# Optimization experiments

Measured on AMD Instinct MI355X. Metric: run time of the kernel, lower is better.

## Reference

```python
import jax, jax.numpy as jnp
import numpy as np

B, T, D, H, DEPTH, FF, NC = 512, 150, 256, 8, 6, 1024, 4
HD = D // H  # head dim = 32


def setup_inputs() -> dict:
    key = jax.random.key(0)
    ks = iter(jax.random.split(key, 64))
    n = lambda shape, s=0.02: jax.random.normal(next(ks), shape, jnp.float32) * s
    return dict(
        token_types=jax.random.randint(next(ks), (B, T), 0, 4, jnp.int32),
        decision_ids=jax.random.randint(next(ks), (B, T), 0, NC, jnp.int32),
        action_vals=jax.random.normal(next(ks), (B, T, 1), jnp.float32),
        dis_vals=jax.random.normal(next(ks), (B, T, 10), jnp.float32),
        v_vals=jax.random.normal(next(ks), (B, T, 3), jnp.float32),
        action_W=n((1, D), 0.5), action_b=n((D,)),
        dis_W=n((10, D), 0.2), dis_b=n((D,)),
        v_W=n((3, D), 0.3), v_b=n((D,)),
        decision_table=n((NC, D)),
        pos_embed=n((1, T + 1, D)), cls_token=n((1, 1, D)),
        qkv_W=n((DEPTH, D, 3 * D), 0.05), qkv_b=jnp.zeros((DEPTH, 3 * D), jnp.float32),
        out_W=n((DEPTH, D, D), 0.05), out_b=jnp.zeros((DEPTH, D), jnp.float32),
        ln1_g=jnp.ones((DEPTH, D), jnp.float32), ln1_b=jnp.zeros((DEPTH, D), jnp.float32),
        ln2_g=jnp.ones((DEPTH, D), jnp.float32), ln2_b=jnp.zeros((DEPTH, D), jnp.float32),
        ffn1_W=n((DEPTH, D, FF), 0.05), ffn1_b=jnp.zeros((DEPTH, FF), jnp.float32),
        ffn2_W=n((DEPTH, FF, D), 0.05), ffn2_b=jnp.zeros((DEPTH, D), jnp.float32),
        dec_ln_g=jnp.ones((D,), jnp.float32), dec_ln_b=jnp.zeros((D,), jnp.float32),
        dec_W=n((D, NC), 0.05), dec_b=jnp.zeros((NC,), jnp.float32),
        act_ln_g=jnp.ones((D,), jnp.float32), act_ln_b=jnp.zeros((D,), jnp.float32),
        act_W=n((D, 1), 0.05), act_b=jnpp if False else jnp.zeros((1,), jnp.float32),
    )


def _ln(x, g, b):
    # PyTorch LayerNorm: eps=1e-5, biased variance
    m = jnp.mean(x, axis=-1, keepdims=True)
    v = jnp.mean(jnp.square(x - m), axis=-1, keepdims=True)
    return (x - m) * jax.lax.rsqrt(v + 1e-5) * g + b


def reference(token_types, decision_ids, action_vals, dis_vals, v_vals,
              action_W, action_b, dis_W, dis_b, v_W, v_b, decision_table,
              pos_embed, cls_token, qkv_W, qkv_b, out_W, out_b,
              ln1_g, ln1_b, ln2_g, ln2_b, ffn1_W, ffn1_b, ffn2_W, ffn2_b,
              dec_ln_g, dec_ln_b, dec_W, dec_b, act_ln_g, act_ln_b, act_W, act_b):
    # --- batched type-dispatched token embedding (replaces the per-token python loop) ---
    a_emb = action_vals @ action_W + action_b                     # [B,T,D] type 'A'
    s_emb = dis_vals @ dis_W + dis_b + v_vals @ v_W + v_b         # [B,T,D] type 'S'
    d_emb = decision_table[decision_ids]                          # [B,T,D] type 'D'
    t = token_types[..., None]
    x = jnp.where(t == 0, a_emb, jnp.where(t == 1, s_emb, jnp.where(t == 2, d_emb, 0.0)))
    # --- prepend CLS, add positional embedding ---
    x = jnp.concatenate([jnp.broadcast_to(cls_token, (x.shape[0], 1, D)), x], axis=1)
    S = x.shape[1]
    x = x + pos_embed[:, :S, :]
    # --- post-norm TransformerEncoder (PyTorch default: ReLU FFN, norm_first=False, eval/no dropout) ---
    scale = 1.0 / np.sqrt(HD).astype(np.float32)
    for i in range(DEPTH):
        qkv = x @ qkv_W[i] + qkv_b[i]                             # [B,S,3D]
        q, k, v = jnp.split(qkv, 3, axis=-1)
        q = q.reshape(-1, S, H, HD)
        k = k.reshape(-1, S, H, HD)
        v = v.reshape(-1, S, H, HD)
        att = jax.nn.softmax(jnp.einsum('bqhd,bkhd->bhqk', q, k) * scale, axis=-1)
        o = jnp.einsum('bhqk,bkhd->bqhd', att, v).reshape(-1, S, D)
        x = _ln(x + o @ out_W[i] + out_b[i], ln1_g[i], ln1_b[i])
        ff = jax.nn.relu(x @ ffn1_W[i] + ffn1_b[i]) @ ffn2_W[i] + ffn2_b[i]
        x = _ln(x + ff, ln2_g[i], ln2_b[i])
    cls = x[:, 0, :]
    decision_logits = _ln(cls, dec_ln_g, dec_ln_b) @ dec_W + dec_b   # [B,4]
    action_pred = _ln(cls, act_ln_g, act_ln_b) @ act_W + act_b       # [B,1]
    return (decision_logits, action_pred)
```

## Files before the change

### kernel.cpp

```cpp
#include <hip/hip_runtime.h>
#include <hip/hip_bf16.h>

typedef __hip_bfloat16 bf16;
typedef unsigned short u16;
typedef __attribute__((ext_vector_type(8))) short s16x8;
typedef __attribute__((ext_vector_type(4))) float f32x4;

#define B_ 512
#define T_ 150
#define S_ 151
#define D_ 256
#define H_ 8
#define HD_ 32
#define FF_ 1024
#define NC_ 4
#define DEPTH_ 6
#define MTOT 77312
#define MT128 (MTOT / 128)
#define MT64 (MTOT / 64)

#define XOFF 0
#define C1OFF (MTOT * D_)
#define C2OFF (C1OFF + MTOT * FF_)
#define WSELEMS (C2OFF + MTOT * D_)

#define QKVT_OFF 0
#define OUTT_OFF (QKVT_OFF + DEPTH_ * D_ * 768)
#define FFN1T_OFF (OUTT_OFF + DEPTH_ * D_ * D_)
#define FFN2T_OFF (FFN1T_OFF + DEPTH_ * D_ * FF_)
#define WTELEMS (FFN2T_OFF + DEPTH_ * FF_ * D_)

__device__ __align__(16) u16 g_ws[WSELEMS];
__device__ __align__(16) u16 g_wt[WTELEMS];
__device__ int g_f32flag;

__device__ __forceinline__ float ldf(const void* p, size_t i, int f) {
  return f ? ((const float*)p)[i] : __bfloat162float(((const bf16*)p)[i]);
}
__device__ __forceinline__ float b2f(u16 u) {
  union { unsigned int i; float f; } v; v.i = ((unsigned int)u) << 16; return v.f;
}
__device__ __forceinline__ u16 f2b(float x) {
  bf16 h = __float2bfloat16(x);
  return *reinterpret_cast<u16*>(&h);
}

typedef __attribute__((address_space(3))) void lds_void;
typedef const __attribute__((address_space(1))) void glob_void;
__device__ __forceinline__ void gload_lds16(const u16* g, u16* l) {
  __builtin_amdgcn_global_load_lds((glob_void*)g, (lds_void*)l, 16, 0, 0);
}

#define PROBE_N 38656
__global__ __launch_bounds__(256) void probe_kernel(const void* pe)
{
  const u16* w = (const u16*)pe;
  int susp = 0, zeroEven = 0;
  for (int k = threadIdx.x; k < PROBE_N; k += 256) {
    u16 u = w[k];
    int ex = (u >> 7) & 0xFF;
    if (ex >= 141) susp++;
    if ((k & 1) == 0 && (u & 0x7FFF) == 0) zeroEven++;
  }
  __shared__ int s_susp, s_zero;
  if (threadIdx.x == 0) { s_susp = 0; s_zero = 0; }
  __syncthreads();
  atomicAdd(&s_susp, susp);
  atomicAdd(&s_zero, zeroEven);
  __syncthreads();
  if (threadIdx.x == 0)
    g_f32flag = (s_susp > 0 || s_zero >= ((PROBE_N / 2) * 9) / 10) ? 1 : 0;
}

__global__ __launch_bounds__(256) void wtrans_kernel(const void* src, int dstOff,
                                                     int K, int N, int total)
{
  const int f = g_f32flag;
  int idx = blockIdx.x * 256 + threadIdx.x;
  if (idx >= total) return;
  int kn = K * N;
  int l = idx / kn;
  int r = idx - l * kn;
  int k = r / N;
  int n = r - k * N;
  g_wt[dstOff + (size_t)l * kn + (size_t)n * K + k] = f2b(ldf(src, idx, f));
}

__global__ __launch_bounds__(256) void embed_kernel(
    const int* __restrict__ tt, const int* __restrict__ dids,
    const void* av, const void* dv, const void* vv,
    const void* aW, const void* ab, const void* dW, const void* db,
    const void* vW, const void* vb, const void* table, const void* pos,
    const void* cls)
{
  const int f = g_f32flag;
  u16* x = g_ws + XOFF;
  int row = blockIdx.x;
  int d = threadIdx.x;
  int b = row / S_;
  int s = row - b * S_;
  float val;
  if (s == 0) {
    val = ldf(cls, d, f);
  } else {
    int t = s - 1;
    int idx = b * T_ + t;
    int ty = tt[idx];
    if (ty == 0) {
      val = ldf(av, idx, f) * ldf(aW, d, f) + ldf(ab, d, f);
    } else if (ty == 1) {
      float acc = ldf(db, d, f) + ldf(vb, d, f);
#pragma unroll
      for (int i = 0; i < 10; i++) acc += ldf(dv, (size_t)idx * 10 + i, f) * ldf(dW, i * D_ + d, f);
#pragma unroll
      for (int i = 0; i < 3; i++) acc += ldf(vv, (size_t)idx * 3 + i, f) * ldf(vW, i * D_ + d, f);
      val = acc;
    } else if (ty == 2) {
      int did = dids[idx] & (NC_ - 1);
      val = ldf(table, (size_t)did * D_ + d, f);
    } else {
      val = 0.f;
    }
  }
  val += ldf(pos, s * D_ + d, f);
  x[(size_t)row * D_ + d] = f2b(val);
}

__global__ __launch_bounds__(256, 3) void gemm_mfma(
    int aOff, int wtOff, const void* bias, size_t bOff,
    int cOff, int N, int K, int relu, int NB)
{
  const int f = g_f32flag;
  const u16* A = g_ws + aOff;
  const u16* Bt = g_wt + wtOff;
  u16* C = g_ws + cOff;
  __shared__ __align__(16) u16 sm[16384];
  const int tid = threadIdx.x;

  int gblk = blockIdx.x;
  int bm, bn;
  {
    const int full = (MT128 / 8) * 8;
    if (gblk < NB * full) {
      int per = NB * 8;
      int grp = gblk / per, rem = gblk % per;
      bm = grp * 8 + (rem & 7);
      bn = rem >> 3;
    } else {
      int id = gblk - NB * full;
      bm = full + id / NB;
      bn = id % NB;
    }
  }

  const int lane = tid & 63, wid = tid >> 6;
  const int wm = (wid >> 1) * 64, wn = (wid & 1) * 64;
  const int frow = lane & 15, quad = lane >> 4;

  const int rg = lane >> 3;
  const int ck = ((lane & 7) ^ rg) * 8;
  const u16* Ag[4]; const u16* Bg[4];
  u16 *Asl[4], *Bsl[4];
#pragma unroll
  for (int p = 0; p < 4; p++) {
    int grp = wid * 4 + p;
    int row = grp * 8 + rg;
    Ag[p] = A + (size_t)(bm * 128 + row) * K + ck;
    Bg[p] = Bt + (size_t)(bn * 128 + row) * K + ck;
    Asl[p] = &sm[grp * 512];
    Bsl[p] = &sm[8192 + grp * 512];
  }

  f32x4 acc[4][4] = {};

  for (int kt = 0; kt < K; kt += 64) {
    if (kt) __syncthreads();
#pragma unroll
    for (int p = 0; p < 4; p++) {
      gload_lds16(Ag[p] + kt, Asl[p]);
      gload_lds16(Bg[p] + kt, Bsl[p]);
    }
    __syncthreads();
#pragma unroll
    for (int s = 0; s < 2; s++) {
      s16x8 af[4], bfr[4];
      const int cfr = ((s * 4 + quad) ^ (frow & 7)) * 8;
#pragma unroll
      for (int t = 0; t < 4; t++) {
        af[t]  = *(const s16x8*)&sm[(wm + t * 16 + frow) * 64 + cfr];
        bfr[t] = *(const s16x8*)&sm[8192 + (wn + t * 16 + frow) * 64 + cfr];
      }
#pragma unroll
      for (int mt = 0; mt < 4; mt++)
#pragma unroll
        for (int nt = 0; nt < 4; nt++)
          acc[mt][nt] = __builtin_amdgcn_mfma_f32_16x16x32_bf16(af[mt], bfr[nt], acc[mt][nt], 0, 0, 0);
    }
  }

  float bv[4];
#pragma unroll
  for (int nt = 0; nt < 4; nt++)
    bv[nt] = ldf(bias, bOff + (size_t)(bn * 128 + wn + nt * 16 + frow), f);
  __syncthreads();
#pragma unroll
  for (int p = 0; p < 2; p++) {
    if ((wid >> 1) == p) {
#pragma unroll
      for (int mt = 0; mt < 4; mt++)
#pragma unroll
        for (int nt = 0; nt < 4; nt++)
#pragma unroll
          for (int r = 0; r < 4; r++) {
            int rl = (wm & 63) + mt * 16 + quad * 4 + r;
            float v = acc[mt][nt][r] + bv[nt];
            if (relu) v = fmaxf(v, 0.f);
            sm[rl * 136 + wn + nt * 16 + frow] = f2b(v);
          }
    }
    __syncthreads();
    {
      int rl = tid >> 2;
      int cq = (tid & 3) * 32;
      size_t gb = (size_t)(bm * 128 + p * 64 + rl) * N + bn * 128 + cq;
#pragma unroll
      for (int j = 0; j < 4; j++)
        *(s16x8*)(C + gb + j * 8) = *(const s16x8*)&sm[rl * 136 + cq + j * 8];
    }
    __syncthreads();
  }
}

#define LNHALF 20480

__global__ __launch_bounds__(256, 2) void gemm_ln(
    int aOff, int wtOff, const void* bias, size_t bOff,
    const void* lng, const void* lnb, size_t lnOff, int K)
{
  const int f = g_f32flag;
  const u16* A = g_ws + aOff;
  const u16* Bt = g_wt + wtOff;
  __shared__ __align__(16) u16 sm[2 * LNHALF];
  const int tid = threadIdx.x;
  const int bm = blockIdx.x;
  const int lane = tid & 63, wid = tid >> 6;
  const int wn = wid * 64;
  const int frow = lane & 15, quad = lane >> 4;
  const int rg = lane >> 3;
  const int ck = ((lane & 7) ^ rg) * 8;

  const u16* Ag[2]; u16* Asl[2];
  const u16* Bg[8]; u16* Bsl[8];
#pragma unroll
  for (int p = 0; p < 2; p++) {
    int grp = wid * 2 + p;
    Ag[p] = A + (size_t)(bm * 64 + grp * 8 + rg) * K + ck;
    Asl[p] = &sm[grp * 512];
  }
#pragma unroll
  for (int p = 0; p < 8; p++) {
    int grp = wid * 8 + p;
    Bg[p] = Bt + (size_t)(grp * 8 + rg) * K + ck;
    Bsl[p] = &sm[4096 + grp * 512];
  }

  f32x4 acc[4][4] = {};
  const int nsteps = K >> 6;

#pragma unroll
  for (int p = 0; p < 2; p++) gload_lds16(Ag[p], Asl[p]);
#pragma unroll
  for (int p = 0; p < 8; p++) gload_lds16(Bg[p], Bsl[p]);
  __syncthreads();

  for (int t = 0; t < nsteps; t++) {
    const int cur = (t & 1) * LNHALF;
    if (t + 1 < nsteps) {
      const int nxt = ((t + 1) & 1) * LNHALF;
      const int kt = (t + 1) << 6;
#pragma unroll
      for (int p = 0; p < 2; p++) gload_lds16(Ag[p] + kt, Asl[p] + nxt);
#pragma unroll
      for (int p = 0; p < 8; p++) gload_lds16(Bg[p] + kt, Bsl[p] + nxt);
    }
#pragma unroll
    for (int s = 0; s < 2; s++) {
      s16x8 af[4], bfr[4];
      const int cfr = ((s * 4 + quad) ^ (frow & 7)) * 8;
#pragma unroll
      for (int ti = 0; ti < 4; ti++) {
        af[ti]  = *(const s16x8*)&sm[cur + (ti * 16 + frow) * 64 + cfr];
        bfr[ti] = *(const s16x8*)&sm[cur + 4096 + (wn + ti * 16 + frow) * 64 + cfr];
      }
#pragma unroll
      for (int mt = 0; mt < 4; mt++)
#pragma unroll
        for (int nt = 0; nt < 4; nt++)
          acc[mt][nt] = __builtin_amdgcn_mfma_f32_16x16x32_bf16(af[mt], bfr[nt], acc[mt][nt], 0, 0, 0);
    }
    __syncthreads();
  }

  const int rl = tid >> 2;
  const int cq = (tid & 3) * 64;
  const size_t rowg = (size_t)bm * 64 + rl;
  s16x8 xr[8];
#pragma unroll
  for (int j = 0; j < 8; j++)
    xr[j] = *(const s16x8*)(g_ws + XOFF + rowg * 256 + cq + j * 8);

  float bv[4];
#pragma unroll
  for (int nt = 0; nt < 4; nt++)
    bv[nt] = ldf(bias, bOff + (size_t)(wn + nt * 16 + frow), f);
#pragma unroll
  for (int mt = 0; mt < 4; mt++)
#pragma unroll
    for (int nt = 0; nt < 4; nt++)
#pragma unroll
      for (int r = 0; r < 4; r++) {
        int row = mt * 16 + quad * 4 + r;
        int col = wn + nt * 16 + frow;
        sm[row * 264 + col] = f2b(acc[mt][nt][r] + bv[nt]);
      }
  __syncthreads();
  {
    float s1 = 0.f, s2 = 0.f;
#pragma unroll
    for (int j = 0; j < 8; j++) {
      s16x8 yv = *(const s16x8*)&sm[rl * 264 + cq + j * 8];
#pragma unroll
      for (int e = 0; e < 8; e++) {
        float v = b2f((u16)yv[e]) + b2f((u16)xr[j][e]);
        s1 += v; s2 += v * v;
      }
    }
    s1 += __shfl_xor(s1, 1, 64); s2 += __shfl_xor(s2, 1, 64);
    s1 += __shfl_xor(s1, 2, 64); s2 += __shfl_xor(s2, 2, 64);
    float mean = s1 * (1.f / 256.f);
    float var = s2 * (1.f / 256.f) - mean * mean;
    float rs = rsqrtf(var + 1e-5f);
#pragma unroll
    for (int j = 0; j < 8; j++) {
      s16x8 yv = *(const s16x8*)&sm[rl * 264 + cq + j * 8];
      s16x8 ov;
#pragma unroll
      for (int e = 0; e < 8; e++) {
        float v = b2f((u16)yv[e]) + b2f((u16)xr[j][e]);
        int col = cq + j * 8 + e;
        ov[e] = (short)f2b((v - mean) * rs * ldf(lng, lnOff + col, f) + ldf(lnb, lnOff + col, f));
      }
      *(s16x8*)(g_ws + XOFF + rowg * 256 + cq + j * 8) = ov;
    }
  }
}

#define SP 160
#define KLD 32
#define VLD 170
#define PLDS 42

__global__ __launch_bounds__(320) void attn_kernel()
{
  const u16* qkv = g_ws + C1OFF;
  u16* o = g_ws + C2OFF;
  __shared__ __align__(16) u16 Ks[SP * KLD];
  __shared__ __align__(16) u16 Vt[HD_ * VLD];
  __shared__ __align__(16) u16 Ps[5][16 * PLDS];
  int bh = blockIdx.x;
  int b = bh >> 3, h = bh & 7;
  int tid = threadIdx.x;
  int lane = tid & 63, wid = tid >> 6;
  const u16* base = qkv + (size_t)b * S_ * 768;

  {
    const int jrow = lane >> 2;
    const int dsw = (((lane & 3) ^ ((lane >> 3) & 3)) * 8);
#pragma unroll
    for (int p = 0; p < 2; p++) {
      int g = wid * 2 + p;
      int j = g * 16 + jrow;
      gload_lds16(base + (size_t)j * 768 + 256 + h * 32 + dsw, &Ks[g * 512]);
    }
  }
  for (int g = tid; g < SP * 4; g += 320) {
    int j = g >> 2, d0 = (g & 3) * 8;
    s16x8 vv = {0, 0, 0, 0, 0, 0, 0, 0};
    if (j < S_) vv = *(const s16x8*)(base + (size_t)j * 768 + 512 + h * 32 + d0);
#pragma unroll
    for (int i = 0; i < 8; i++) Vt[(d0 + i) * VLD + j] = (u16)vv[i];
  }
  __syncthreads();

  const int frow = lane & 15;
  const int quad = lane >> 4;
  const int fk = quad * 8;
  const float scale = 0.17677669529663687f;
  u16* Pw = &Ps[wid][0];

  for (int round = 0; round < 2; round++) {
    int mt = round * 5 + wid;
    int qrow = mt * 16 + frow;
    s16x8 aq = {0, 0, 0, 0, 0, 0, 0, 0};
    if (qrow < S_) aq = *(const s16x8*)(base + (size_t)qrow * 768 + h * 32 + fk);
    f32x4 sacc[10];
#pragma unroll
    for (int nt = 0; nt < 10; nt++) {
      s16x8 bk = *(const s16x8*)&Ks[(nt * 16 + frow) * KLD
                                    + ((quad ^ ((frow >> 1) & 3)) * 8)];
      f32x4 z = {0.f, 0.f, 0.f, 0.f};
      sacc[nt] = __builtin_amdgcn_mfma_f32_16x16x32_bf16(aq, bk, z, 0, 0, 0);
    }
#pragma unroll
    for (int nt = 0; nt < 10; nt++) {
      int colg = nt * 16 + frow;
      float msk = (colg < S_) ? 1.f : 0.f;
#pragma unroll
      for (int r = 0; r < 4; r++)
        sacc[nt][r] = msk ? sacc[nt][r] * scale : -1e30f;
    }
    float inv[4];
#pragma unroll
    for (int r = 0; r < 4; r++) {
      float mx = -1e30f;
#pragma unroll
      for (int nt = 0; nt < 10; nt++) mx = fmaxf(mx, sacc[nt][r]);
#pragma unroll
      for (int m = 1; m < 16; m <<= 1) mx = fmaxf(mx, __shfl_xor(mx, m, 64));
      float sm2 = 0.f;
#pragma unroll
      for (int nt = 0; nt < 10; nt++) {
        float p = __expf(sacc[nt][r] - mx);
        sacc[nt][r] = p;
        sm2 += p;
      }
#pragma unroll
      for (int m = 1; m < 16; m <<= 1) sm2 += __shfl_xor(sm2, m, 64);
      inv[r] = 1.f / sm2;
    }
    f32x4 oacc[2] = {};
#pragma unroll
    for (int ks = 0; ks < 5; ks++) {
#pragma unroll
      for (int h2 = 0; h2 < 2; h2++) {
        int nt = ks * 2 + h2;
#pragma unroll
        for (int r = 0; r < 4; r++)
          Pw[(quad * 4 + r) * PLDS + h2 * 16 + frow] = f2b(sacc[nt][r]);
      }
      s16x8 ap = *(const s16x8*)&Pw[frow * PLDS + fk];
#pragma unroll
      for (int nt2 = 0; nt2 < 2; nt2++) {
        s16x8 bv = *(const s16x8*)&Vt[(nt2 * 16 + frow) * VLD + ks * 32 + fk];
        oacc[nt2] = __builtin_amdgcn_mfma_f32_16x16x32_bf16(ap, bv, oacc[nt2], 0, 0, 0);
      }
    }
#pragma unroll
    for (int nt2 = 0; nt2 < 2; nt2++)
#pragma unroll
      for (int r = 0; r < 4; r++) {
        int rowg = mt * 16 + quad * 4 + r;
        if (rowg < S_)
          o[(size_t)(b * S_ + rowg) * D_ + h * 32 + nt2 * 16 + frow] = f2b(oacc[nt2][r] * inv[r]);
      }
  }
}

__global__ __launch_bounds__(256) void head_kernel(
    const void* dg, const void* dbt, const void* dW, const void* dbias,
    const void* ag, const void* abt, const void* aW, const void* abias,
    void* out)
{
  const int f = g_f32flag;
  const u16* x = g_ws + XOFF;
  int bg = blockIdx.x;
  int tid = threadIdx.x;
  float c = b2f(x[(size_t)bg * S_ * D_ + tid]);
  float s1 = c, s2 = c * c;
#pragma unroll
  for (int off = 32; off > 0; off >>= 1) {
    s1 += __shfl_down(s1, off, 64);
    s2 += __shfl_down(s2, off, 64);
  }
  __shared__ float ws1[4], ws2[4], stats[2];
  __shared__ float lnD[256], lnA[256];
  int wid = tid >> 6, lane = tid & 63;
  if (lane == 0) { ws1[wid] = s1; ws2[wid] = s2; }
  __syncthreads();
  if (tid == 0) {
    float t1 = ws1[0] + ws1[1] + ws1[2] + ws1[3];
    float t2 = ws2[0] + ws2[1] + ws2[2] + ws2[3];
    float mean = t1 * (1.f / 256.f);
    float var = t2 * (1.f / 256.f) - mean * mean;
    stats[0] = mean;
    stats[1] = rsqrtf(var + 1e-5f);
  }
  __syncthreads();
  float n = (c - stats[0]) * stats[1];
  lnD[tid] = n * ldf(dg, tid, f) + ldf(dbt, tid, f);
  lnA[tid] = n * ldf(ag, tid, f) + ldf(abt, tid, f);
  __syncthreads();
  if (tid < NC_) {
    float acc = ldf(dbias, tid, f);
    for (int k = 0; k < D_; k++) acc += lnD[k] * ldf(dW, k * NC_ + tid, f);
    if (f) ((float*)out)[bg * NC_ + tid] = acc;
    else   ((bf16*)out)[bg * NC_ + tid] = __float2bfloat16(acc);
  } else if (tid == 8) {
    float acc = ldf(abias, 0, f);
    for (int k = 0; k < D_; k++) acc += lnA[k] * ldf(aW, k, f);
    if (f) ((float*)out)[B_ * NC_ + bg] = acc;
    else   ((bf16*)out)[B_ * NC_ + bg] = __float2bfloat16(acc);
  }
}

extern "C" void kernel_launch(void* const* d_in, const int* in_sizes, int n_in,
                              void* d_out, int out_size, void* d_ws, size_t ws_size,
                              hipStream_t stream)
{
  (void)in_sizes; (void)out_size; (void)d_ws; (void)ws_size;
  if (n_in < 34) return;
  const int* token_types  = (const int*)d_in[0];
  const int* decision_ids = (const int*)d_in[1];

  probe_kernel<<<1, 256, 0, stream>>>(d_in[12]);

  wtrans_kernel<<<(DEPTH_ * D_ * 768 + 255) / 256, 256, 0, stream>>>(
      d_in[14], QKVT_OFF, D_, 768, DEPTH_ * D_ * 768);
  wtrans_kernel<<<(DEPTH_ * D_ * D_ + 255) / 256, 256, 0, stream>>>(
      d_in[16], OUTT_OFF, D_, D_, DEPTH_ * D_ * D_);
  wtrans_kernel<<<(DEPTH_ * D_ * FF_ + 255) / 256, 256, 0, stream>>>(
      d_in[22], FFN1T_OFF, D_, FF_, DEPTH_ * D_ * FF_);
  wtrans_kernel<<<(DEPTH_ * FF_ * D_ + 255) / 256, 256, 0, stream>>>(
      d_in[24], FFN2T_OFF, FF_, D_, DEPTH_ * FF_ * D_);

  embed_kernel<<<MTOT, 256, 0, stream>>>(token_types, decision_ids,
      d_in[2], d_in[3], d_in[4], d_in[5], d_in[6], d_in[7], d_in[8],
      d_in[9], d_in[10], d_in[11], d_in[12], d_in[13]);

  for (int i = 0; i < DEPTH_; i++) {
    gemm_mfma<<<6 * MT128, 256, 0, stream>>>(XOFF,
        QKVT_OFF + i * D_ * 768, d_in[15], (size_t)i * 768, C1OFF, 768, D_, 0, 6);
    attn_kernel<<<B_ * H_, 320, 0, stream>>>();
    gemm_ln<<<MT64, 256, 0, stream>>>(C2OFF,
        OUTT_OFF + i * D_ * D_, d_in[17], (size_t)i * D_,
        d_in[18], d_in[19], (size_t)i * D_, D_);
    gemm_mfma<<<8 * MT128, 256, 0, stream>>>(XOFF,
        FFN1T_OFF + i * D_ * FF_, d_in[23], (size_t)i * FF_, C1OFF, FF_, D_, 1, 8);
    gemm_ln<<<MT64, 256, 0, stream>>>(C1OFF,
        FFN2T_OFF + i * FF_ * D_, d_in[25], (size_t)i * D_,
        d_in[20], d_in[21], (size_t)i * D_, FF_);
  }
  head_kernel<<<B_, 256, 0, stream>>>(d_in[26], d_in[27], d_in[28], d_in[29],
      d_in[30], d_in[31], d_in[32], d_in[33], d_out);
}
```

Baseline: 2.532 ms.

## Enlarge LayerNorm GEMM tile to 128 rows with 8 waves, single-buffered LDS

The fused GEMM+LayerNorm kernel now has each block cover 128 rows using 512 threads in a 2x4 wave grid, where before it covered 64 rows with 4 waves. Each weight tile is reused across twice as many rows, and the grid is halved. The double-buffered prefetch is replaced by a single LDS buffer with sync-load-sync per K step, which cuts LDS use but removes overlap between loads and MFMA. An extra barrier is added before the epilogue writes into the shared buffer that the K loop also uses.

```diff
diff --git a/kernel.cpp b/kernel.cpp
--- a/kernel.cpp
+++ b/kernel.cpp
@@ -231,66 +231,55 @@
   }
 }
 
-#define LNHALF 20480
-
-__global__ __launch_bounds__(256, 2) void gemm_ln(
+__global__ __launch_bounds__(512, 4) void gemm_ln(
     int aOff, int wtOff, const void* bias, size_t bOff,
     const void* lng, const void* lnb, size_t lnOff, int K)
 {
   const int f = g_f32flag;
   const u16* A = g_ws + aOff;
   const u16* Bt = g_wt + wtOff;
-  __shared__ __align__(16) u16 sm[2 * LNHALF];
+  __shared__ __align__(16) u16 sm[33792];
   const int tid = threadIdx.x;
   const int bm = blockIdx.x;
   const int lane = tid & 63, wid = tid >> 6;
-  const int wn = wid * 64;
+  const int wm = (wid >> 2) * 64;
+  const int wn = (wid & 3) * 64;
   const int frow = lane & 15, quad = lane >> 4;
   const int rg = lane >> 3;
   const int ck = ((lane & 7) ^ rg) * 8;
 
   const u16* Ag[2]; u16* Asl[2];
-  const u16* Bg[8]; u16* Bsl[8];
+  const u16* Bg[4]; u16* Bsl[4];
 #pragma unroll
   for (int p = 0; p < 2; p++) {
     int grp = wid * 2 + p;
-    Ag[p] = A + (size_t)(bm * 64 + grp * 8 + rg) * K + ck;
+    Ag[p] = A + (size_t)(bm * 128 + grp * 8 + rg) * K + ck;
     Asl[p] = &sm[grp * 512];
   }
 #pragma unroll
-  for (int p = 0; p < 8; p++) {
-    int grp = wid * 8 + p;
+  for (int p = 0; p < 4; p++) {
+    int grp = wid * 4 + p;
     Bg[p] = Bt + (size_t)(grp * 8 + rg) * K + ck;
-    Bsl[p] = &sm[4096 + grp * 512];
+    Bsl[p] = &sm[8192 + grp * 512];
   }
 
   f32x4 acc[4][4] = {};
-  const int nsteps = K >> 6;
-
-#pragma unroll
-  for (int p = 0; p < 2; p++) gload_lds16(Ag[p], Asl[p]);
-#pragma unroll
-  for (int p = 0; p < 8; p++) gload_lds16(Bg[p], Bsl[p]);
-  __syncthreads();
-
-  for (int t = 0; t < nsteps; t++) {
-    const int cur = (t & 1) * LNHALF;
-    if (t + 1 < nsteps) {
-      const int nxt = ((t + 1) & 1) * LNHALF;
-      const int kt = (t + 1) << 6;
-#pragma unroll
-      for (int p = 0; p < 2; p++) gload_lds16(Ag[p] + kt, Asl[p] + nxt);
-#pragma unroll
-      for (int p = 0; p < 8; p++) gload_lds16(Bg[p] + kt, Bsl[p] + nxt);
-    }
+
+  for (int kt = 0; kt < K; kt += 64) {
+    if (kt) __syncthreads();
+#pragma unroll
+    for (int p = 0; p < 2; p++) gload_lds16(Ag[p] + kt, Asl[p]);
+#pragma unroll
+    for (int p = 0; p < 4; p++) gload_lds16(Bg[p] + kt, Bsl[p]);
+    __syncthreads();
 #pragma unroll
     for (int s = 0; s < 2; s++) {
       s16x8 af[4], bfr[4];
       const int cfr = ((s * 4 + quad) ^ (frow & 7)) * 8;
 #pragma unroll
       for (int ti = 0; ti < 4; ti++) {
-        af[ti]  = *(const s16x8*)&sm[cur + (ti * 16 + frow) * 64 + cfr];
-        bfr[ti] = *(const s16x8*)&sm[cur + 4096 + (wn + ti * 16 + frow) * 64 + cfr];
+        af[ti]  = *(const s16x8*)&sm[(wm + ti * 16 + frow) * 64 + cfr];
+        bfr[ti] = *(const s16x8*)&sm[8192 + (wn + ti * 16 + frow) * 64 + cfr];
       }
 #pragma unroll
       for (int mt = 0; mt < 4; mt++)
@@ -298,12 +287,11 @@
         for (int nt = 0; nt < 4; nt++)
           acc[mt][nt] = __builtin_amdgcn_mfma_f32_16x16x32_bf16(af[mt], bfr[nt], acc[mt][nt], 0, 0, 0);
     }
-    __syncthreads();
   }
 
   const int rl = tid >> 2;
   const int cq = (tid & 3) * 64;
-  const size_t rowg = (size_t)bm * 64 + rl;
+  const size_t rowg = (size_t)bm * 128 + rl;
   s16x8 xr[8];
 #pragma unroll
   for (int j = 0; j < 8; j++)
@@ -313,13 +301,14 @@
 #pragma unroll
   for (int nt = 0; nt < 4; nt++)
     bv[nt] = ldf(bias, bOff + (size_t)(wn + nt * 16 + frow), f);
+  __syncthreads();
 #pragma unroll
   for (int mt = 0; mt < 4; mt++)
 #pragma unroll
     for (int nt = 0; nt < 4; nt++)
 #pragma unroll
       for (int r = 0; r < 4; r++) {
-        int row = mt * 16 + quad * 4 + r;
+        int row = wm + mt * 16 + quad * 4 + r;
         int col = wn + nt * 16 + frow;
         sm[row * 264 + col] = f2b(acc[mt][nt][r] + bv[nt]);
       }
@@ -541,12 +530,12 @@
     gemm_mfma<<<6 * MT128, 256, 0, stream>>>(XOFF,
         QKVT_OFF + i * D_ * 768, d_in[15], (size_t)i * 768, C1OFF, 768, D_, 0, 6);
     attn_kernel<<<B_ * H_, 320, 0, stream>>>();
-    gemm_ln<<<MT64, 256, 0, stream>>>(C2OFF,
+    gemm_ln<<<MT128, 512, 0, stream>>>(C2OFF,
         OUTT_OFF + i * D_ * D_, d_in[17], (size_t)i * D_,
         d_in[18], d_in[19], (size_t)i * D_, D_);
     gemm_mfma<<<8 * MT128, 256, 0, stream>>>(XOFF,
         FFN1T_OFF + i * D_ * FF_, d_in[23], (size_t)i * FF_, C1OFF, FF_, D_, 1, 8);
-    gemm_ln<<<MT64, 256, 0, stream>>>(C1OFF,
+    gemm_ln<<<MT128, 512, 0, stream>>>(C1OFF,
         FFN2T_OFF + i * FF_ * D_, d_in[25], (size_t)i * D_,
         d_in[20], d_in[21], (size_t)i * D_, FF_);
   }
```

Measured after the change: 2.930 ms. 1.16x slower.

## Store GEMM-LN A operands in 64x64 tiled layout for contiguous loads

Applied to the files above, without the earlier changes.

The FFN1 GEMM output and the attention output are now written in a 64x64-tiled layout, each tile 4096 contiguous elements. The gemm_ln kernel reads its A operand with matching tiled addressing, so each 64x64 K-step chunk is one contiguous 8 KB block instead of 64 strided rows. This is meant to improve DRAM and TLB locality for the large activation reads. The attention kernel's scattered 2-byte stores get a more complex address computation, and every producer and consumer must agree on the layout.

```diff
diff --git a/kernel.cpp b/kernel.cpp
--- a/kernel.cpp
+++ b/kernel.cpp
@@ -128,7 +128,7 @@
 
 __global__ __launch_bounds__(256, 3) void gemm_mfma(
     int aOff, int wtOff, const void* bias, size_t bOff,
-    int cOff, int N, int K, int relu, int NB)
+    int cOff, int N, int K, int relu, int NB, int tiledC)
 {
   const int f = g_f32flag;
   const u16* A = g_ws + aOff;
@@ -222,10 +222,20 @@
     {
       int rl = tid >> 2;
       int cq = (tid & 3) * 32;
-      size_t gb = (size_t)(bm * 128 + p * 64 + rl) * N + bn * 128 + cq;
-#pragma unroll
-      for (int j = 0; j < 4; j++)
-        *(s16x8*)(C + gb + j * 8) = *(const s16x8*)&sm[rl * 136 + cq + j * 8];
+      if (!tiledC) {
+        size_t gb = (size_t)(bm * 128 + p * 64 + rl) * N + bn * 128 + cq;
+#pragma unroll
+        for (int j = 0; j < 4; j++)
+          *(s16x8*)(C + gb + j * 8) = *(const s16x8*)&sm[rl * 136 + cq + j * 8];
+      } else {
+        const size_t tmBase = (size_t)(bm * 2 + p) * (N >> 6);
+#pragma unroll
+        for (int j = 0; j < 4; j++) {
+          int col = bn * 128 + cq + j * 8;
+          size_t addr = ((tmBase + (col >> 6)) << 12) + (rl << 6) + (col & 63);
+          *(s16x8*)(C + addr) = *(const s16x8*)&sm[rl * 136 + cq + j * 8];
+        }
+      }
     }
     __syncthreads();
   }
@@ -254,7 +264,7 @@
 #pragma unroll
   for (int p = 0; p < 2; p++) {
     int grp = wid * 2 + p;
-    Ag[p] = A + (size_t)(bm * 64 + grp * 8 + rg) * K + ck;
+    Ag[p] = A + ((size_t)bm * (K >> 6) << 12) + ((grp * 8 + rg) << 6) + ck;
     Asl[p] = &sm[grp * 512];
   }
 #pragma unroll
@@ -277,11 +287,12 @@
     const int cur = (t & 1) * LNHALF;
     if (t + 1 < nsteps) {
       const int nxt = ((t + 1) & 1) * LNHALF;
-      const int kt = (t + 1) << 6;
-#pragma unroll
-      for (int p = 0; p < 2; p++) gload_lds16(Ag[p] + kt, Asl[p] + nxt);
-#pragma unroll
-      for (int p = 0; p < 8; p++) gload_lds16(Bg[p] + kt, Bsl[p] + nxt);
+      const int ktA = (t + 1) << 12;
+      const int ktB = (t + 1) << 6;
+#pragma unroll
+      for (int p = 0; p < 2; p++) gload_lds16(Ag[p] + ktA, Asl[p] + nxt);
+#pragma unroll
+      for (int p = 0; p < 8; p++) gload_lds16(Bg[p] + ktB, Bsl[p] + nxt);
     }
 #pragma unroll
     for (int s = 0; s < 2; s++) {
@@ -460,8 +471,12 @@
 #pragma unroll
       for (int r = 0; r < 4; r++) {
         int rowg = mt * 16 + quad * 4 + r;
-        if (rowg < S_)
-          o[(size_t)(b * S_ + rowg) * D_ + h * 32 + nt2 * 16 + frow] = f2b(oacc[nt2][r] * inv[r]);
+        if (rowg < S_) {
+          int gr = b * S_ + rowg;
+          int gc = h * 32 + nt2 * 16 + frow;
+          o[(((size_t)(gr >> 6) * (D_ >> 6) + (gc >> 6)) << 12)
+            + ((gr & 63) << 6) + (gc & 63)] = f2b(oacc[nt2][r] * inv[r]);
+        }
       }
   }
 }
@@ -539,13 +554,13 @@
 
   for (int i = 0; i < DEPTH_; i++) {
     gemm_mfma<<<6 * MT128, 256, 0, stream>>>(XOFF,
-        QKVT_OFF + i * D_ * 768, d_in[15], (size_t)i * 768, C1OFF, 768, D_, 0, 6);
+        QKVT_OFF + i * D_ * 768, d_in[15], (size_t)i * 768, C1OFF, 768, D_, 0, 6, 0);
     attn_kernel<<<B_ * H_, 320, 0, stream>>>();
     gemm_ln<<<MT64, 256, 0, stream>>>(C2OFF,
         OUTT_OFF + i * D_ * D_, d_in[17], (size_t)i * D_,
         d_in[18], d_in[19], (size_t)i * D_, D_);
     gemm_mfma<<<8 * MT128, 256, 0, stream>>>(XOFF,
-        FFN1T_OFF + i * D_ * FF_, d_in[23], (size_t)i * FF_, C1OFF, FF_, D_, 1, 8);
+        FFN1T_OFF + i * D_ * FF_, d_in[23], (size_t)i * FF_, C1OFF, FF_, D_, 1, 8, 1);
     gemm_ln<<<MT64, 256, 0, stream>>>(C1OFF,
         FFN2T_OFF + i * FF_ * D_, d_in[25], (size_t)i * D_,
         d_in[20], d_in[21], (size_t)i * D_, FF_);
```

Result: faster. 2.480 ms (-2.1%).
